# Kernel tuning notes

Hardware: AMD Instinct MI355X
Metric: run time of the kernel (lower is better)

## Reference

```python
import jax, jax.numpy as jnp
import numpy as np

EPS = 1e-5
K = 20
UP = 2

def _knn_idx(x, k):
    # x: (B, C, N) -> idx: (B, N, k) of nearest neighbors by squared L2
    inner = -2.0 * jnp.einsum('bcn,bcm->bnm', x, x)
    xx = jnp.sum(x * x, axis=1)  # (B, N)
    pd = -xx[:, :, None] - inner - xx[:, None, :]  # negative squared distance
    _, idx = jax.lax.top_k(pd, k)
    return idx

def _bn(x, g, b, m, v):
    # eval-mode BatchNorm2d over channel axis 1 of (B, C, N, k)
    scale = g / jnp.sqrt(v + EPS)
    return x * scale[None, :, None, None] + (b - m * scale)[None, :, None, None]

def _lrelu(x):
    return jnp.where(x >= 0, x, 0.2 * x)

def setup_inputs() -> dict:
    key = jax.random.key(0)
    ks = jax.random.split(key, 13)
    B, N, C = 16, 2048, 64
    return {
        'xyz': jax.random.normal(ks[0], (B, 3, N), dtype=jnp.float32),
        'xyz_f': jax.random.normal(ks[1], (B, C, N), dtype=jnp.float32),
        'W1': jax.random.normal(ks[2], (32, 128), dtype=jnp.float32) * 0.1,
        'g1': jax.random.uniform(ks[3], (32,), dtype=jnp.float32),
        'b1': jax.random.normal(ks[4], (32,), dtype=jnp.float32),
        'm1': jax.random.normal(ks[5], (32,), dtype=jnp.float32),
        'v1': jax.random.uniform(ks[6], (32,), dtype=jnp.float32),
        'W2': jax.random.normal(ks[7], (32, 32), dtype=jnp.float32) * 0.1,
        'g2': jax.random.uniform(ks[8], (32,), dtype=jnp.float32),
        'b2': jax.random.normal(ks[9], (32,), dtype=jnp.float32),
        'm2': jax.random.normal(ks[10], (32,), dtype=jnp.float32),
        'v2': jax.random.uniform(ks[11], (32,), dtype=jnp.float32),
        'W3': jax.random.normal(ks[12], (64, 32), dtype=jnp.float32) * 0.1,
    }

def reference(xyz, xyz_f, W1, g1, b1, m1, v1, W2, g2, b2, m2, v2, W3):
    B, C, N = xyz_f.shape
    idx = _knn_idx(xyz, K)  # (B, N, K)
    xf = jnp.transpose(xyz_f, (0, 2, 1))  # (B, N, C)
    # gather neighbor features: (B, N, K, C)
    nbr = xf[jnp.arange(B)[:, None, None], idx]
    edge = jnp.concatenate([nbr - xf[:, :, None, :],
                            jnp.broadcast_to(xf[:, :, None, :], (B, N, K, C))], axis=-1)
    f = jnp.transpose(edge, (0, 3, 1, 2))  # (B, 2C, N, K)
    f = _lrelu(_bn(jnp.einsum('oc,bcnk->bonk', W1, f), g1, b1, m1, v1))
    f = _lrelu(_bn(jnp.einsum('oc,bcnk->bonk', W2, f), g2, b2, m2, v2))
    f = jnp.einsum('oc,bcnk->bonk', W3, f)  # (B, 64, N, K)
    f = jnp.max(f, axis=-1)  # (B, 64, N)
    # point_shuffler(scale=2): (B, 64, N) -> (B, 32, 2N)
    Bc, Cc, Nc = f.shape
    f = jnp.transpose(f, (0, 2, 1)).reshape(Bc, Nc, UP, Cc // UP)
    f = f.reshape(Bc, Nc * UP, Cc // UP)
    return jnp.transpose(f, (0, 2, 1))
```

## Files before the change

kernel.cpp:

```cpp
#include <hip/hip_runtime.h>
#include <cstdint>
#include <math.h>

#define NPTS 2048
#define NBATCH 16
#define KNBR 20

#define OFF_YT   0u
#define OFF_W1AF 2097152u
#define OFF_W1BF 2099200u
#define OFF_B1F  2101248u
#define OFF_W2F  2101280u
#define OFF_B2F  2102304u
#define OFF_IDX  2102336u

__global__ void fold_kernel(const float* __restrict__ W1, const float* __restrict__ g1,
                            const float* __restrict__ b1, const float* __restrict__ m1,
                            const float* __restrict__ v1, const float* __restrict__ W2,
                            const float* __restrict__ g2, const float* __restrict__ b2,
                            const float* __restrict__ m2, const float* __restrict__ v2,
                            float* __restrict__ W1AF, float* __restrict__ W1BF,
                            float* __restrict__ B1F, float* __restrict__ W2F,
                            float* __restrict__ B2F) {
  const int o = threadIdx.x;
  if (o < 32) {
    const float s1 = g1[o] / sqrtf(v1[o] + 1e-5f);
    const float s2 = g2[o] / sqrtf(v2[o] + 1e-5f);
    B1F[o] = b1[o] - m1[o] * s1;
    B2F[o] = b2[o] - m2[o] * s2;
    for (int c = 0; c < 64; ++c) {
      W1AF[o * 64 + c] = W1[o * 128 + c] * s1;
      W1BF[o * 64 + c] = W1[o * 128 + 64 + c] * s1;
    }
    for (int c = 0; c < 32; ++c) W2F[o * 32 + c] = W2[o * 32 + c] * s2;
  }
}

__global__ __launch_bounds__(256) void pre_kernel(const float* __restrict__ xf,
                                                  const float* __restrict__ W1AF,
                                                  const float* __restrict__ W1BF,
                                                  const float* __restrict__ B1F,
                                                  float* __restrict__ yt) {
  const int p = blockIdx.x * 256 + threadIdx.x;
  const int b = p >> 11, n = p & 2047;
  const float* src = xf + (size_t)b * 64 * NPTS + n;
  float cen[64];
#pragma unroll
  for (int c = 0; c < 64; ++c) cen[c] = src[(size_t)c * NPTS];
  float y[32], t1[32];
#pragma unroll
  for (int o = 0; o < 32; ++o) {
    float a = 0.f;
    float bb = B1F[o];
#pragma unroll
    for (int c = 0; c < 64; ++c) {
      a = fmaf(W1AF[o * 64 + c], cen[c], a);
      bb = fmaf(W1BF[o * 64 + c], cen[c], bb);
    }
    y[o] = a;
    t1[o] = bb - a;
  }
  float* dst = yt + (size_t)p * 64;
#pragma unroll
  for (int o = 0; o < 32; o += 4) {
    *(float4*)(dst + o) = make_float4(y[o], y[o + 1], y[o + 2], y[o + 3]);
    *(float4*)(dst + 32 + o) = make_float4(t1[o], t1[o + 1], t1[o + 2], t1[o + 3]);
  }
}

__device__ __forceinline__ float pd_of(const float4 qp, const float nqxx, const float4 c) {
  const float dot = __fadd_rn(__fadd_rn(__fmul_rn(qp.x, c.x), __fmul_rn(qp.y, c.y)),
                              __fmul_rn(qp.z, c.z));
  return __fsub_rn(__fadd_rn(nqxx, __fmul_rn(2.0f, dot)), c.w);
}

__global__ __launch_bounds__(256, 3) void knn_kernel(const float* __restrict__ xyz,
                                                     int* __restrict__ knn_out) {
  __shared__ float4 spt[NPTS];
  __shared__ int qlist[256 * KNBR];
  const int b = blockIdx.x >> 5;
  const int qbase = (blockIdx.x & 31) << 6;
  const int tid = threadIdx.x;
  const float* src = xyz + (size_t)b * 3 * NPTS;
  for (int i = tid; i < NPTS; i += 256) {
    const float x = src[i], y = src[NPTS + i], z = src[2 * NPTS + i];
    const float xx = __fadd_rn(__fadd_rn(__fmul_rn(x, x), __fmul_rn(y, y)), __fmul_rn(z, z));
    spt[i] = make_float4(x, y, z, xx);
  }
  __syncthreads();

  const int q = qbase + (tid & 63);
  const int quad = tid >> 6;
  const float4 qp = spt[q];
  const float nqxx = -qp.w;
  const int j0 = quad << 9, j1 = j0 + 512;

  float arr[KNBR];
#pragma unroll
  for (int s = 0; s < KNBR; ++s) arr[s] = -INFINITY;
  for (int j = j0; j < j1; ++j) {
    float v = pd_of(qp, nqxx, spt[j]);
#pragma unroll
    for (int s = 0; s < KNBR; ++s) {
      const float hi = fmaxf(arr[s], v);
      v = fminf(arr[s], v);
      arr[s] = hi;
    }
  }
  const float T = arr[KNBR - 1];
  int cnt = 0;
  int* myq = qlist + tid * KNBR;
  for (int j = j0; j < j1; ++j) {
    const float pd = pd_of(qp, nqxx, spt[j]);
    if (pd >= T && cnt < KNBR) { myq[cnt] = j; ++cnt; }
  }
  __syncthreads();

  if (tid < 64) {
    float bpd[KNBR];
    int bidx[KNBR];
#pragma unroll
    for (int s = 0; s < KNBR; ++s) { bpd[s] = -INFINITY; bidx[s] = 0; }
    const float4 qp2 = spt[qbase + tid];
    const float nq2 = -qp2.w;
    for (int quad2 = 0; quad2 < 4; ++quad2) {
      for (int jj = 0; jj < KNBR; ++jj) {
        const int id = qlist[((quad2 << 6) | tid) * KNBR + jj];
        const float v = pd_of(qp2, nq2, spt[id]);
        if (v > bpd[KNBR - 1]) {
#pragma unroll
          for (int s = KNBR - 1; s >= 1; --s) {
            const bool c1 = v > bpd[s - 1];
            const float pj = c1 ? bpd[s - 1] : v;
            const int ij = c1 ? bidx[s - 1] : id;
            if (v > bpd[s]) { bpd[s] = pj; bidx[s] = ij; }
          }
          if (v > bpd[0]) { bpd[0] = v; bidx[0] = id; }
        }
      }
    }
    int* dst = knn_out + ((size_t)(b * NPTS + qbase + tid)) * KNBR;
#pragma unroll
    for (int s = 0; s < KNBR; ++s) dst[s] = bidx[s];
  }
}

__global__ __launch_bounds__(256, 2) void mlp_kernel(const float* __restrict__ ws,
                                                     const int* __restrict__ knn,
                                                     const float* __restrict__ W3,
                                                     float* __restrict__ out) {
  const int t = blockIdx.x * 256 + threadIdx.x;
  const int p = t >> 2;
  const int kq = t & 3;
  const int b = p >> 11;
  const int n = p & 2047;
  const float* __restrict__ yt = ws + OFF_YT;
  const float* __restrict__ W2 = ws + OFF_W2F;
  const float* __restrict__ B2 = ws + OFF_B2F;
  const float* __restrict__ ybase = yt + ((size_t)(b << 11)) * 64;

  float t1c[32];
  {
    const float* tp = yt + (size_t)p * 64 + 32;
#pragma unroll
    for (int o = 0; o < 32; o += 4) {
      const float4 v = *(const float4*)(tp + o);
      t1c[o] = v.x; t1c[o + 1] = v.y; t1c[o + 2] = v.z; t1c[o + 3] = v.w;
    }
  }
  float hmax[64];
#pragma unroll
  for (int o = 0; o < 64; ++o) hmax[o] = -INFINITY;

#pragma unroll 1
  for (int kk = 0; kk < 5; ++kk) {
    const int nb = knn[p * KNBR + kq * 5 + kk] & 2047;
    const float* __restrict__ yp = ybase + (size_t)nb * 64;

    float h1[32];
#pragma unroll
    for (int o = 0; o < 32; o += 4) {
      const float4 v = *(const float4*)(yp + o);
      h1[o] = t1c[o] + v.x;
      h1[o + 1] = t1c[o + 1] + v.y;
      h1[o + 2] = t1c[o + 2] + v.z;
      h1[o + 3] = t1c[o + 3] + v.w;
    }
#pragma unroll
    for (int o = 0; o < 32; ++o) h1[o] = fmaxf(h1[o], 0.2f * h1[o]);

    float h2[32];
#pragma unroll
    for (int o = 0; o < 32; ++o) {
      float a = B2[o];
#pragma unroll
      for (int c = 0; c < 32; ++c) a = fmaf(W2[o * 32 + c], h1[c], a);
      h2[o] = fmaxf(a, 0.2f * a);
    }
#pragma unroll
    for (int o = 0; o < 64; ++o) {
      float a = 0.f;
#pragma unroll
      for (int c = 0; c < 32; ++c) a = fmaf(W3[o * 32 + c], h2[c], a);
      hmax[o] = fmaxf(hmax[o], a);
    }
  }
#pragma unroll
  for (int o = 0; o < 64; ++o) {
    hmax[o] = fmaxf(hmax[o], __shfl_xor(hmax[o], 1));
    hmax[o] = fmaxf(hmax[o], __shfl_xor(hmax[o], 2));
  }
  if (kq == 0) {
    float* op = out + (size_t)b * (32 * 4096) + 2 * n;
#pragma unroll
    for (int f = 0; f < 64; ++f) {
      const int u = f >> 5, cc = f & 31;
      op[cc * 4096 + u] = hmax[f];
    }
  }
}

extern "C" void kernel_launch(void* const* d_in, const int* in_sizes, int n_in,
                              void* d_out, int out_size, void* d_ws, size_t ws_size,
                              hipStream_t stream) {
  const float* xyz = (const float*)d_in[0];
  const float* xyz_f = (const float*)d_in[1];
  const float* W1 = (const float*)d_in[2];
  const float* g1 = (const float*)d_in[3];
  const float* b1 = (const float*)d_in[4];
  const float* m1 = (const float*)d_in[5];
  const float* v1 = (const float*)d_in[6];
  const float* W2 = (const float*)d_in[7];
  const float* g2 = (const float*)d_in[8];
  const float* b2 = (const float*)d_in[9];
  const float* m2 = (const float*)d_in[10];
  const float* v2 = (const float*)d_in[11];
  const float* W3 = (const float*)d_in[12];
  float* ws = (float*)d_ws;
  float* out = (float*)d_out;
  int* knn = (int*)(ws + OFF_IDX);

  fold_kernel<<<1, 64, 0, stream>>>(W1, g1, b1, m1, v1, W2, g2, b2, m2, v2,
                                    ws + OFF_W1AF, ws + OFF_W1BF, ws + OFF_B1F,
                                    ws + OFF_W2F, ws + OFF_B2F);
  pre_kernel<<<128, 256, 0, stream>>>(xyz_f, ws + OFF_W1AF, ws + OFF_W1BF, ws + OFF_B1F,
                                      ws + OFF_YT);
  knn_kernel<<<512, 256, 0, stream>>>(xyz, knn);
  mlp_kernel<<<512, 256, 0, stream>>>(ws, knn, W3, out);
}
```

Before: 640.1 us.

## Split KNN scan into eight slices and halve MLP output channels per thread

The KNN kernel now uses 512 threads per block, so each query is scanned by eight 256-point slices instead of four 512-point slices, and the final merge combines eight candidate lists. The MLP kernel assigns each point to eight threads, with each thread computing half of the 64 output channels, which cuts the per-thread register footprint and doubles the grid. W2 and W3 are repacked into interleaved pairs so float2 loads can be used, and the neighbour loop is fully unrolled. The trade-off is more redundant layer-2 work per thread, a longer serial merge in the KNN tail, and larger shared memory per block.

Result: slower. 1.409 ms (+120.1%).

```diff
diff --git a/kernel.cpp b/kernel.cpp
--- a/kernel.cpp
+++ b/kernel.cpp
@@ -10,18 +10,20 @@
 #define OFF_W1AF 2097152u
 #define OFF_W1BF 2099200u
 #define OFF_B1F  2101248u
-#define OFF_W2F  2101280u
-#define OFF_B2F  2102304u
-#define OFF_IDX  2102336u
+#define OFF_B2F  2101280u
+#define OFF_W2P  2101312u
+#define OFF_W3P  2103360u
+#define OFF_IDX  2105408u
 
 __global__ void fold_kernel(const float* __restrict__ W1, const float* __restrict__ g1,
                             const float* __restrict__ b1, const float* __restrict__ m1,
                             const float* __restrict__ v1, const float* __restrict__ W2,
                             const float* __restrict__ g2, const float* __restrict__ b2,
                             const float* __restrict__ m2, const float* __restrict__ v2,
+                            const float* __restrict__ W3,
                             float* __restrict__ W1AF, float* __restrict__ W1BF,
-                            float* __restrict__ B1F, float* __restrict__ W2F,
-                            float* __restrict__ B2F) {
+                            float* __restrict__ B1F, float* __restrict__ B2F,
+                            float* __restrict__ W2P, float* __restrict__ W3P) {
   const int o = threadIdx.x;
   if (o < 32) {
     const float s1 = g1[o] / sqrtf(v1[o] + 1e-5f);
@@ -32,7 +34,12 @@
       W1AF[o * 64 + c] = W1[o * 128 + c] * s1;
       W1BF[o * 64 + c] = W1[o * 128 + 64 + c] * s1;
     }
-    for (int c = 0; c < 32; ++c) W2F[o * 32 + c] = W2[o * 32 + c] * s2;
+    for (int c = 0; c < 32; ++c)
+      W2P[(((o >> 1) << 5) + c) * 2 + (o & 1)] = W2[o * 32 + c] * s2;
+  }
+  if (o < 64) {
+    for (int c = 0; c < 32; ++c)
+      W3P[(((o >> 1) << 5) + c) * 2 + (o & 1)] = W3[o * 32 + c];
   }
 }
 
@@ -74,15 +81,15 @@
   return __fsub_rn(__fadd_rn(nqxx, __fmul_rn(2.0f, dot)), c.w);
 }
 
-__global__ __launch_bounds__(256, 3) void knn_kernel(const float* __restrict__ xyz,
+__global__ __launch_bounds__(512, 4) void knn_kernel(const float* __restrict__ xyz,
                                                      int* __restrict__ knn_out) {
   __shared__ float4 spt[NPTS];
-  __shared__ int qlist[256 * KNBR];
+  __shared__ int qlist[512 * KNBR];
   const int b = blockIdx.x >> 5;
   const int qbase = (blockIdx.x & 31) << 6;
   const int tid = threadIdx.x;
   const float* src = xyz + (size_t)b * 3 * NPTS;
-  for (int i = tid; i < NPTS; i += 256) {
+  for (int i = tid; i < NPTS; i += 512) {
     const float x = src[i], y = src[NPTS + i], z = src[2 * NPTS + i];
     const float xx = __fadd_rn(__fadd_rn(__fmul_rn(x, x), __fmul_rn(y, y)), __fmul_rn(z, z));
     spt[i] = make_float4(x, y, z, xx);
@@ -90,10 +97,10 @@
   __syncthreads();
 
   const int q = qbase + (tid & 63);
-  const int quad = tid >> 6;
+  const int slice = tid >> 6;
   const float4 qp = spt[q];
   const float nqxx = -qp.w;
-  const int j0 = quad << 9, j1 = j0 + 512;
+  const int j0 = slice << 8, j1 = j0 + 256;
 
   float arr[KNBR];
 #pragma unroll
@@ -123,9 +130,9 @@
     for (int s = 0; s < KNBR; ++s) { bpd[s] = -INFINITY; bidx[s] = 0; }
     const float4 qp2 = spt[qbase + tid];
     const float nq2 = -qp2.w;
-    for (int quad2 = 0; quad2 < 4; ++quad2) {
+    for (int s2 = 0; s2 < 8; ++s2) {
       for (int jj = 0; jj < KNBR; ++jj) {
-        const int id = qlist[((quad2 << 6) | tid) * KNBR + jj];
+        const int id = qlist[((s2 << 6) | tid) * KNBR + jj];
         const float v = pd_of(qp2, nq2, spt[id]);
         if (v > bpd[KNBR - 1]) {
 #pragma unroll
@@ -145,18 +152,19 @@
   }
 }
 
-__global__ __launch_bounds__(256, 2) void mlp_kernel(const float* __restrict__ ws,
+__global__ __launch_bounds__(256, 4) void mlp_kernel(const float* __restrict__ ws,
                                                      const int* __restrict__ knn,
-                                                     const float* __restrict__ W3,
                                                      float* __restrict__ out) {
   const int t = blockIdx.x * 256 + threadIdx.x;
-  const int p = t >> 2;
-  const int kq = t & 3;
+  const int p = t >> 3;
+  const int kq = (t >> 1) & 3;
+  const int oh = t & 1;
   const int b = p >> 11;
   const int n = p & 2047;
   const float* __restrict__ yt = ws + OFF_YT;
-  const float* __restrict__ W2 = ws + OFF_W2F;
-  const float* __restrict__ B2 = ws + OFF_B2F;
+  const float* __restrict__ W2P = ws + OFF_W2P;
+  const float* __restrict__ W3P = ws + OFF_W3P;
+  const float* __restrict__ B2F = ws + OFF_B2F;
   const float* __restrict__ ybase = yt + ((size_t)(b << 11)) * 64;
 
   float t1c[32];
@@ -168,11 +176,11 @@
       t1c[o] = v.x; t1c[o + 1] = v.y; t1c[o + 2] = v.z; t1c[o + 3] = v.w;
     }
   }
-  float hmax[64];
-#pragma unroll
-  for (int o = 0; o < 64; ++o) hmax[o] = -INFINITY;
-
-#pragma unroll 1
+  float2 hm2[16];
+#pragma unroll
+  for (int j = 0; j < 16; ++j) hm2[j] = make_float2(-INFINITY, -INFINITY);
+
+#pragma unroll
   for (int kk = 0; kk < 5; ++kk) {
     const int nb = knn[p * KNBR + kq * 5 + kk] & 2047;
     const float* __restrict__ yp = ybase + (size_t)nb * 64;
@@ -189,33 +197,58 @@
 #pragma unroll
     for (int o = 0; o < 32; ++o) h1[o] = fmaxf(h1[o], 0.2f * h1[o]);
 
+    float2 a2[16];
+#pragma unroll
+    for (int o2 = 0; o2 < 16; ++o2) a2[o2] = *(const float2*)(B2F + 2 * o2);
+#pragma unroll
+    for (int c = 0; c < 32; ++c) {
+      const float hc = h1[c];
+#pragma unroll
+      for (int o2 = 0; o2 < 16; ++o2) {
+        const float2 w = *(const float2*)(W2P + ((((o2 << 5) + c)) << 1));
+        a2[o2].x = fmaf(w.x, hc, a2[o2].x);
+        a2[o2].y = fmaf(w.y, hc, a2[o2].y);
+      }
+    }
     float h2[32];
 #pragma unroll
-    for (int o = 0; o < 32; ++o) {
-      float a = B2[o];
-#pragma unroll
-      for (int c = 0; c < 32; ++c) a = fmaf(W2[o * 32 + c], h1[c], a);
-      h2[o] = fmaxf(a, 0.2f * a);
-    }
-#pragma unroll
-    for (int o = 0; o < 64; ++o) {
-      float a = 0.f;
-#pragma unroll
-      for (int c = 0; c < 32; ++c) a = fmaf(W3[o * 32 + c], h2[c], a);
-      hmax[o] = fmaxf(hmax[o], a);
-    }
-  }
-#pragma unroll
-  for (int o = 0; o < 64; ++o) {
-    hmax[o] = fmaxf(hmax[o], __shfl_xor(hmax[o], 1));
-    hmax[o] = fmaxf(hmax[o], __shfl_xor(hmax[o], 2));
+    for (int o2 = 0; o2 < 16; ++o2) {
+      h2[2 * o2] = fmaxf(a2[o2].x, 0.2f * a2[o2].x);
+      h2[2 * o2 + 1] = fmaxf(a2[o2].y, 0.2f * a2[o2].y);
+    }
+
+    float2 c2[16];
+#pragma unroll
+    for (int j = 0; j < 16; ++j) c2[j] = make_float2(0.f, 0.f);
+#pragma unroll
+    for (int c = 0; c < 32; ++c) {
+      const float hc = h2[c];
+#pragma unroll
+      for (int j = 0; j < 16; ++j) {
+        const float2 w = *(const float2*)(W3P + (((((oh << 4) + j) << 5) + c) << 1));
+        c2[j].x = fmaf(w.x, hc, c2[j].x);
+        c2[j].y = fmaf(w.y, hc, c2[j].y);
+      }
+    }
+#pragma unroll
+    for (int j = 0; j < 16; ++j) {
+      hm2[j].x = fmaxf(hm2[j].x, c2[j].x);
+      hm2[j].y = fmaxf(hm2[j].y, c2[j].y);
+    }
+  }
+#pragma unroll
+  for (int j = 0; j < 16; ++j) {
+    hm2[j].x = fmaxf(hm2[j].x, __shfl_xor(hm2[j].x, 2));
+    hm2[j].y = fmaxf(hm2[j].y, __shfl_xor(hm2[j].y, 2));
+    hm2[j].x = fmaxf(hm2[j].x, __shfl_xor(hm2[j].x, 4));
+    hm2[j].y = fmaxf(hm2[j].y, __shfl_xor(hm2[j].y, 4));
   }
   if (kq == 0) {
-    float* op = out + (size_t)b * (32 * 4096) + 2 * n;
-#pragma unroll
-    for (int f = 0; f < 64; ++f) {
-      const int u = f >> 5, cc = f & 31;
-      op[cc * 4096 + u] = hmax[f];
+    float* op = out + (size_t)b * (32 * 4096) + 2 * n + oh;
+#pragma unroll
+    for (int j = 0; j < 16; ++j) {
+      op[(2 * j) * 4096] = hm2[j].x;
+      op[(2 * j + 1) * 4096] = hm2[j].y;
     }
   }
 }
@@ -240,11 +273,11 @@
   float* out = (float*)d_out;
   int* knn = (int*)(ws + OFF_IDX);
 
-  fold_kernel<<<1, 64, 0, stream>>>(W1, g1, b1, m1, v1, W2, g2, b2, m2, v2,
+  fold_kernel<<<1, 64, 0, stream>>>(W1, g1, b1, m1, v1, W2, g2, b2, m2, v2, W3,
                                     ws + OFF_W1AF, ws + OFF_W1BF, ws + OFF_B1F,
-                                    ws + OFF_W2F, ws + OFF_B2F);
+                                    ws + OFF_B2F, ws + OFF_W2P, ws + OFF_W3P);
   pre_kernel<<<128, 256, 0, stream>>>(xyz_f, ws + OFF_W1AF, ws + OFF_W1BF, ws + OFF_B1F,
                                       ws + OFF_YT);
-  knn_kernel<<<512, 256, 0, stream>>>(xyz, knn);
-  mlp_kernel<<<512, 256, 0, stream>>>(ws, knn, W3, out);
-}
+  knn_kernel<<<512, 512, 0, stream>>>(xyz, knn);
+  mlp_kernel<<<1024, 256, 0, stream>>>(ws, knn, out);
+}
```
